# Kernel optimization log

Measured on AMD Instinct MI355X. Metric: run time of the kernel, lower is better.

The kernel has to match this reference:

```python
import jax, jax.numpy as jnp
import numpy as np

N_HEADS = 16
NOPE = 128
ROPE = 64
VDIM = 128
HEAD_DIM = NOPE + ROPE  # 192


def apply_rope(x, cos, sin):
    # x: [B, S, H, D] with D even; pairs (a, b) rotated by complex freqs.
    B, S, H, D = x.shape
    xr = x.reshape(B, S, H, D // 2, 2)
    a, b = xr[..., 0], xr[..., 1]
    c = cos[None, :, None, :]
    s = sin[None, :, None, :]
    out = jnp.stack([a * c - b * s, a * s + b * c], axis=-1)
    return out.reshape(B, S, H, D)


def setup_inputs() -> dict:
    key = jax.random.key(0)
    ks = jax.random.split(key, 8)
    B, S, DIM = 1, 2048, 2048
    x = jax.random.normal(ks[0], (B, S, DIM), dtype=jnp.float32)
    wq = jax.random.normal(ks[1], (N_HEADS * HEAD_DIM, DIM), dtype=jnp.float32) * (DIM ** -0.5)
    wk = jax.random.normal(ks[2], (N_HEADS * HEAD_DIM, DIM), dtype=jnp.float32) * (DIM ** -0.5)
    wv = jax.random.normal(ks[3], (N_HEADS * VDIM, DIM), dtype=jnp.float32) * (DIM ** -0.5)
    wo = jax.random.normal(ks[4], (DIM, N_HEADS * VDIM), dtype=jnp.float32) * ((N_HEADS * VDIM) ** -0.5)
    # rotary freqs: theta = 10000^{-2i/d}, angles = pos * theta
    inv_freq = 1.0 / (10000.0 ** (np.arange(0, ROPE, 2, dtype=np.float32) / ROPE))
    angles = np.arange(S, dtype=np.float32)[:, None] * inv_freq[None, :]  # [S, 32]
    freqs_cos = jnp.asarray(np.cos(angles))
    freqs_sin = jnp.asarray(np.sin(angles))
    # additive causal mask
    mask = jnp.where(jnp.triu(jnp.ones((S, S), dtype=bool), k=1), -1e9, 0.0).astype(jnp.float32)
    return {"x": x, "wq": wq, "wk": wk, "wv": wv, "wo": wo,
            "freqs_cos": freqs_cos, "freqs_sin": freqs_sin, "mask": mask, "start_pos": 0}


def reference(x, wq, wk, wv, wo, freqs_cos, freqs_sin, mask, start_pos):
    B, S, DIM = x.shape
    q = (x @ wq.T).reshape(B, S, N_HEADS, HEAD_DIM)
    k = (x @ wk.T).reshape(B, S, N_HEADS, HEAD_DIM)
    v = (x @ wv.T).reshape(B, S, N_HEADS, VDIM)
    q_nope, q_pe = q[..., :NOPE], q[..., NOPE:]
    k_nope, k_pe = k[..., :NOPE], k[..., NOPE:]
    q_pe = apply_rope(q_pe, freqs_cos, freqs_sin)
    k_pe = apply_rope(k_pe, freqs_cos, freqs_sin)
    scores = (jnp.einsum('bshd,bthd->bsht', q_nope, k_nope)
              + jnp.einsum('bshd,bthd->bsht', q_pe, k_pe)) * (HEAD_DIM ** -0.5)
    scores = scores + mask[None, :, None, :]
    probs = jax.nn.softmax(scores.astype(jnp.float32), axis=-1).astype(x.dtype)
    out = jnp.einsum('bsht,bthd->bshd', probs, v)
    return out.reshape(B, S, N_HEADS * VDIM) @ wo.T
```

## Files before the change

### kernel.cpp

```cpp
#include <hip/hip_runtime.h>
#include <hip/hip_bf16.h>
#include <math.h>

#define NH 16
#define NOPE 128
#define ROPE 64
#define VDIM 128
#define HD 192
#define SEQ 2048
#define DIM 2048
#define QKD (NH * HD)
#define VD  (NH * VDIM)
#define QKVS 8192

typedef __attribute__((ext_vector_type(8))) short short8;
typedef __attribute__((ext_vector_type(4))) short short4v;
typedef __attribute__((ext_vector_type(4))) float f32x4;
typedef unsigned int u32;

#define WAIT_VM8  0x0F78
#define WAIT_VM6  0x0F76
#define WAIT_VM4  0x0F74
#define WAIT_VM0  0x0F70
#define WAIT_LGKM 0xC07F

static __device__ inline short f2bf(float f) {
  union { float f; unsigned u; } v; v.f = f;
  unsigned r = (v.u + 0x7fffu + ((v.u >> 16) & 1u)) >> 16;
  return (short)r;
}
static __device__ inline float bf2f(unsigned short u) {
  union { unsigned u; float f; } v; v.u = ((unsigned)u) << 16;
  return v.f;
}

static __device__ __forceinline__ void gload16(const short* g, short* l) {
  __builtin_amdgcn_global_load_lds(
      (const __attribute__((address_space(1))) u32*)g,
      (__attribute__((address_space(3))) u32*)l, 16, 0, 0);
}


#define RDA(pp, hh, mh) do { \
  const char* Lb_ = Lsm + ((pp) * 32768) + ((hh) * 16384) + aoff; \
  afr[0] = *(const short8*)(Lb_ + ((mh) * 4096) + 0); \
  afr[1] = *(const short8*)(Lb_ + ((mh) * 4096) + 1024); \
  afr[2] = *(const short8*)(Lb_ + ((mh) * 4096) + 2048); \
  afr[3] = *(const short8*)(Lb_ + ((mh) * 4096) + 3072); \
} while (0)

#define RDB(pp, hh) do { \
  const char* Lb_ = Lsm + 65536 + ((pp) * 32768) + ((hh) * 16384) + boff; \
  bfr[0] = *(const short8*)(Lb_ + 0); \
  bfr[1] = *(const short8*)(Lb_ + 1024); \
  bfr[2] = *(const short8*)(Lb_ + 2048); \
  bfr[3] = *(const short8*)(Lb_ + 3072); \
} while (0)

#define SA(kt, h) do { \
  char* d_ = Lsm + (((kt) & 1) * 32768) + ((h) * 16384) + wv * 1024; \
  gload16(gA0 + (kt) * 64 + (h) * 32, (short*)d_); \
  gload16(gA1 + (kt) * 64 + (h) * 32, (short*)(d_ + 8192)); \
} while (0)

#define SB(kt, h) do { \
  char* d_ = Lsm + 65536 + (((kt) & 1) * 32768) + ((h) * 16384) + wv * 1024; \
  gload16(gB0 + (kt) * 64 + (h) * 32, (short*)d_); \
  gload16(gB1 + (kt) * 64 + (h) * 32, (short*)(d_ + 8192)); \
} while (0)

#define MFMA1(mi, ni) \
  acc[mi][ni] = __builtin_amdgcn_mfma_f32_16x16x32_bf16(afr[(mi) & 3], bfr[ni], acc[mi][ni], 0, 0, 0)

#define MM(mh) do { \
  MFMA1((mh)*4+0, 0); MFMA1((mh)*4+1, 0); MFMA1((mh)*4+2, 0); MFMA1((mh)*4+3, 0); \
  MFMA1((mh)*4+0, 1); MFMA1((mh)*4+1, 1); MFMA1((mh)*4+2, 1); MFMA1((mh)*4+3, 1); \
  MFMA1((mh)*4+0, 2); MFMA1((mh)*4+1, 2); MFMA1((mh)*4+2, 2); MFMA1((mh)*4+3, 2); \
  MFMA1((mh)*4+0, 3); MFMA1((mh)*4+1, 3); MFMA1((mh)*4+2, 3); MFMA1((mh)*4+3, 3); \
} while (0)

#define GBAR() __builtin_amdgcn_s_barrier()
#define GLGKM0() __builtin_amdgcn_s_waitcnt(WAIT_LGKM)
#define GPRIO1() __builtin_amdgcn_s_setprio(1)
#define GPRIO0() __builtin_amdgcn_s_setprio(0)
#define GNOP ((void)0)

#define TILE(pp, S1, S2, S3, S4, VMW) do { \
  RDA(pp, 0, 0); RDB(pp, 0); S1; \
  GBAR(); GLGKM0(); GPRIO1(); MM(0); GPRIO0(); GBAR(); \
  RDA(pp, 0, 1); S2; \
  GBAR(); GLGKM0(); GPRIO1(); MM(1); GPRIO0(); GBAR(); \
  RDA(pp, 1, 0); RDB(pp, 1); S3; \
  GBAR(); GLGKM0(); GPRIO1(); MM(0); GPRIO0(); GBAR(); \
  RDA(pp, 1, 1); S4; \
  GBAR(); GLGKM0(); GPRIO1(); MM(1); GPRIO0(); VMW; GBAR(); \
} while (0)

__global__ __launch_bounds__(512, 2) void gemm256_bt(
    const short* __restrict__ A, const short* __restrict__ B,
    short* __restrict__ C, int K, int lda, int ldb, int ldc) {
  __shared__ __align__(16) char Lsm[131072];

  const int tid = threadIdx.x;
  const int lane = tid & 63;
  const int l15 = lane & 15;
  const int quad = lane >> 4;
  const int wv = tid >> 6;
  const int wr = wv >> 2, wc = wv & 3;

  const int bid = blockIdx.x;
  const int swz = (bid & 7) * 32 + (bid >> 3);
  const int m0 = (swz >> 5) * 256;
  const int n0 = (swz & 31) * 256;

  const short* gA0 = A + (size_t)(m0 + wv * 16 + l15) * lda + quad * 8;
  const short* gA1 = gA0 + (size_t)128 * lda;
  const short* gB0 = B + (size_t)(n0 + wv * 16 + l15) * ldb + quad * 8;
  const short* gB1 = gB0 + (size_t)128 * ldb;

  const int aoff = wr * 8192 + lane * 16;
  const int boff = wc * 4096 + lane * 16;

  f32x4 acc[8][4];
#pragma unroll
  for (int i = 0; i < 8; ++i)
#pragma unroll
    for (int j = 0; j < 4; ++j) acc[i][j] = (f32x4)(0.f);
  short8 afr[4], bfr[4];

  const int NT = K >> 6;

  SB(0, 0); SA(0, 0); SB(0, 1); SA(0, 1);
  SB(1, 0); SA(1, 0); SB(1, 1);
  __builtin_amdgcn_s_waitcnt(WAIT_VM6);
  GBAR();

  int kt = 0;
  for (; kt + 4 <= NT; kt += 2) {
    TILE(0, SA(kt + 1, 1), SB(kt + 2, 0), SA(kt + 2, 0), SB(kt + 2, 1),
         __builtin_amdgcn_s_waitcnt(WAIT_VM6));
    TILE(1, SA(kt + 2, 1), SB(kt + 3, 0), SA(kt + 3, 0), SB(kt + 3, 1),
         __builtin_amdgcn_s_waitcnt(WAIT_VM6));
  }
  TILE(0, SA(kt + 1, 1), GNOP, GNOP, GNOP, __builtin_amdgcn_s_waitcnt(WAIT_VM0));
  TILE(1, GNOP, GNOP, GNOP, GNOP, GNOP);

#pragma unroll
  for (int m = 0; m < 8; ++m) {
    const size_t rb = (size_t)(m0 + wr * 128 + m * 16 + quad * 4) * ldc +
                      n0 + wc * 64 + l15;
#pragma unroll
    for (int n = 0; n < 4; ++n)
#pragma unroll
      for (int r = 0; r < 4; ++r)
        C[rb + (size_t)r * ldc + n * 16] = f2bf(acc[m][n][r]);
  }
}

template <bool BF16OUT>
__global__ __launch_bounds__(256) void gemm_bt(
    const short* __restrict__ A, const short* __restrict__ B,
    void* __restrict__ Cv, int K, int lda, int ldb, int ldc, float oscale) {
  __shared__ __align__(16) short Ls[4][2][4096];

  const int tid = threadIdx.x;
  const int lane = tid & 63;
  const int wave = tid >> 6;
  const int wr = wave >> 1, wc = wave & 1;
  const int lane15 = lane & 15, quad = lane >> 4;
  const int m0 = blockIdx.y * 128, n0 = blockIdx.x * 128;

  const short* gA[4]; const short* gB[4];
#pragma unroll
  for (int i = 0; i < 4; ++i) {
    int gidx = i * 64 + lane;
    int r = gidx >> 2, p = gidx & 3;
    int g = (p ^ ((r >> 1) & 3)) * 8;
    gA[i] = A + (size_t)(m0 + wr * 64 + r) * lda + g;
    gB[i] = B + (size_t)(n0 + wc * 64 + r) * ldb + g;
  }

  f32x4 acc[4][4];
#pragma unroll
  for (int i = 0; i < 4; ++i)
#pragma unroll
    for (int j = 0; j < 4; ++j) acc[i][j] = (f32x4)(0.f);

#pragma unroll
  for (int i = 0; i < 4; ++i) gload16(gA[i], &Ls[wave][0][i * 512]);
#pragma unroll
  for (int i = 0; i < 4; ++i) gload16(gB[i], &Ls[wave][0][2048 + i * 512]);

  const int rsw = (lane15 >> 1) & 3;
  for (int k0 = 0; k0 < K; k0 += 32) {
    const int cur = (k0 >> 5) & 1;
    __builtin_amdgcn_s_waitcnt(WAIT_LGKM);
    if (k0 + 32 < K) {
      const int nxt = cur ^ 1;
#pragma unroll
      for (int i = 0; i < 4; ++i) gload16(gA[i] + k0 + 32, &Ls[wave][nxt][i * 512]);
#pragma unroll
      for (int i = 0; i < 4; ++i) gload16(gB[i] + k0 + 32, &Ls[wave][nxt][2048 + i * 512]);
      __builtin_amdgcn_s_waitcnt(WAIT_VM8);
    } else {
      __builtin_amdgcn_s_waitcnt(WAIT_VM0);
    }
    const short* bufp = &Ls[wave][cur][0];
    short8 af[4], bfv[4];
#pragma unroll
    for (int i = 0; i < 4; ++i)
      af[i] = *(const short8*)&bufp[(i * 16 + lane15) * 32 + (quad ^ rsw) * 8];
#pragma unroll
    for (int j = 0; j < 4; ++j)
      bfv[j] = *(const short8*)&bufp[2048 + (j * 16 + lane15) * 32 + (quad ^ rsw) * 8];
#pragma unroll
    for (int i = 0; i < 4; ++i)
#pragma unroll
      for (int j = 0; j < 4; ++j)
        acc[i][j] = __builtin_amdgcn_mfma_f32_16x16x32_bf16(af[i], bfv[j], acc[i][j], 0, 0, 0);
  }

#pragma unroll
  for (int i = 0; i < 4; ++i)
#pragma unroll
    for (int j = 0; j < 4; ++j)
#pragma unroll
      for (int r = 0; r < 4; ++r) {
        size_t idx = (size_t)(m0 + wr * 64 + i * 16 + quad * 4 + r) * ldc +
                     n0 + wc * 64 + j * 16 + lane15;
        if (BF16OUT)
          ((short*)Cv)[idx] = f2bf(acc[i][j][r] * oscale);
        else
          ((float*)Cv)[idx] = acc[i][j][r];
      }
}

__global__ __launch_bounds__(256) void rope_qk(
    short* __restrict__ qk, const float* __restrict__ cosf, const float* __restrict__ sinf) {
  int idx = blockIdx.x * blockDim.x + threadIdx.x;
  int j = idx & 31;
  int h = (idx >> 5) & (NH - 1);
  int s = idx >> 9;
  if (s >= SEQ) return;

  float c = cosf[s * 32 + j];
  float sn = sinf[s * 32 + j];
  size_t rowb = (size_t)s * QKVS + h * HD + NOPE + 2 * j;

  u32* pq = (u32*)(qk + rowb);
  u32 w = *pq;
  float a = bf2f((unsigned short)(w & 0xffff));
  float b = bf2f((unsigned short)(w >> 16));
  *pq = (u32)(unsigned short)f2bf(a * c - b * sn) |
        ((u32)(unsigned short)f2bf(a * sn + b * c) << 16);

  u32* pk = (u32*)(qk + rowb + QKD);
  w = *pk;
  a = bf2f((unsigned short)(w & 0xffff));
  b = bf2f((unsigned short)(w >> 16));
  *pk = (u32)(unsigned short)f2bf(a * c - b * sn) |
        ((u32)(unsigned short)f2bf(a * sn + b * c) << 16);
}

__global__ __launch_bounds__(256) void bf16_convert(
    const float* __restrict__ in, short* __restrict__ out, int n4) {
  int i = blockIdx.x * 256 + threadIdx.x;
  if (i >= n4) return;
  float4 f = ((const float4*)in)[i];
  short4v o;
  o.x = f2bf(f.x); o.y = f2bf(f.y); o.z = f2bf(f.z); o.w = f2bf(f.w);
  ((short4v*)out)[i] = o;
}

__global__ __launch_bounds__(256) void conv_wqkv(
    const float* __restrict__ wq, const float* __restrict__ wk,
    const float* __restrict__ wv, short* __restrict__ wqkv, int n4) {
  int i = blockIdx.x * 256 + threadIdx.x;
  if (i >= n4) return;
  int row = i >> 9;
  float4 f;
  if (row < QKD) f = ((const float4*)wq)[i];
  else if (row < 2 * QKD) f = ((const float4*)wk)[i - QKD * (DIM / 4)];
  else f = ((const float4*)wv)[i - 2 * QKD * (DIM / 4)];
  short4v o;
  o.x = f2bf(f.x); o.y = f2bf(f.y); o.z = f2bf(f.z); o.w = f2bf(f.w);
  ((short4v*)wqkv)[i] = o;
}

__global__ __launch_bounds__(256) void vt_bf16(
    const short* __restrict__ vb, short* __restrict__ vtb) {
  __shared__ short tile[64][74];
  const int t0 = blockIdx.x * 64;
  const int c0 = blockIdx.y * 64;
  const int tid = threadIdx.x;
#pragma unroll
  for (int i = 0; i < 16; ++i) {
    int idx = i * 256 + tid;
    int r = idx >> 6, c = idx & 63;
    tile[r][c] = vb[(size_t)(t0 + r) * QKVS + c0 + c];
  }
  __syncthreads();
  const int h = c0 >> 7;
  const int dbase = c0 & 127;
#pragma unroll
  for (int i = 0; i < 16; ++i) {
    int idx = i * 256 + tid;
    int d = idx >> 6, t = idx & 63;
    vtb[(size_t)h * VDIM * SEQ + (size_t)(dbase + d) * SEQ + t0 + t] = tile[t][d];
  }
}

#define BQ 64
#define BT 64
#define CHT 8
#define PSTR 76
#define MFIX 8.0f

__global__ __launch_bounds__(256) void attn_part(
    const short* __restrict__ qk,
    const short* __restrict__ vtb,
    short* __restrict__ Opart,
    float* __restrict__ lpart)
{
  __shared__ __align__(16) short Ks[2][BT * 192];
  __shared__ __align__(16) short Vt[VDIM * 64];
  __shared__ __align__(16) short Ps[4 * 16 * PSTR];

  const int bid = blockIdx.x;
  const int i0 = bid >> 3;
  const int h = (bid & 7) + ((i0 >> 7) << 3);
  const int qt = (i0 & 127) >> 2;
  const int chk = i0 & 3;
  if (chk * CHT > qt) return;

  const int tid = threadIdx.x;
  const int wave = tid >> 6;
  const int lane = tid & 63;
  const int lane15 = lane & 15;
  const int quad = lane >> 4;
  const int bb = qt >> 3;
  const int slot = h * 80 + qt + 4 * bb * (bb - 1) + (qt - 8 * bb) * bb + chk;
  const int R0 = qt * BQ;
  const int kt_beg = chk * CHT;
  const int kt_end = min(kt_beg + CHT, qt + 1);
  const float scale = 0.072168784f;

  const int qrow = R0 + wave * 16 + lane15;
  short8 qf[6];
  const short* qbase = qk + (size_t)qrow * QKVS + h * HD + quad * 8;
#pragma unroll
  for (int kc = 0; kc < 6; ++kc) qf[kc] = *(const short8*)(qbase + kc * 32);
  __builtin_amdgcn_sched_barrier(0);

  const short* kb = qk + QKD;
  int lKoff[6]; const short* gK[6];
#pragma unroll
  for (int i = 0; i < 6; ++i) {
    int id = i * 256 + tid;
    int row = id / 24, cX = id - row * 24;
    int ch = cX ^ (row & 7);
    lKoff[i] = id * 8;
    gK[i] = kb + (size_t)row * QKVS + h * HD + ch * 8;
  }
  const short* gV[4]; short* lV[4];
#pragma unroll
  for (int i = 0; i < 4; ++i) {
    int id = i * 256 + tid;
    int row = id >> 3, cX = id & 7;
    int ch = cX ^ (row & 7);
    lV[i] = &Vt[id * 8];
    gV[i] = vtb + (size_t)h * VDIM * SEQ + (size_t)row * SEQ + ch * 8;
  }

  f32x4 oacc[8];
#pragma unroll
  for (int i = 0; i < 8; ++i) oacc[i] = (f32x4)(0.f);
  float lsum[4] = {0.f, 0.f, 0.f, 0.f};

  short* pw = &Ps[wave * 16 * PSTR];

  {
    const size_t t0 = (size_t)kt_beg * BT;
#pragma unroll
    for (int i = 0; i < 6; ++i) gload16(gK[i] + t0 * QKVS, &Ks[0][lKoff[i]]);
#pragma unroll
    for (int i = 0; i < 4; ++i) gload16(gV[i] + t0, lV[i]);
  }
  __builtin_amdgcn_s_waitcnt(WAIT_VM0);
  __builtin_amdgcn_s_barrier();
  __builtin_amdgcn_sched_barrier(0);

  for (int kt = kt_beg; kt < kt_end; ++kt) {
    const int cur = (kt - kt_beg) & 1;
    const bool have = (kt + 1 < kt_end);

    if (have) {
      const size_t tn = (size_t)(kt + 1) * BT;
#pragma unroll
      for (int i = 0; i < 6; ++i) gload16(gK[i] + tn * QKVS, &Ks[cur ^ 1][lKoff[i]]);
    }

    const short* kcur = &Ks[cur][0];
    f32x4 sacc[4];
    __builtin_amdgcn_s_setprio(1);
#pragma unroll
    for (int c = 0; c < 4; ++c) {
      sacc[c] = (f32x4)(0.f);
      const int row = c * 16 + lane15;
#pragma unroll
      for (int kc = 0; kc < 6; ++kc) {
        int cX = (4 * kc + quad) ^ (lane15 & 7);
        short8 kf = *(const short8*)&kcur[row * 192 + cX * 8];
        sacc[c] = __builtin_amdgcn_mfma_f32_16x16x32_bf16(qf[kc], kf, sacc[c], 0, 0, 0);
      }
    }
    __builtin_amdgcn_s_setprio(0);

    if (kt == qt) {
#pragma unroll
      for (int c = 0; c < 4; ++c)
#pragma unroll
        for (int r = 0; r < 4; ++r) {
          int tloc = c * 16 + lane15;
          int qloc = wave * 16 + quad * 4 + r;
          if (tloc > qloc) sacc[c][r] = -1e30f;
        }
    }

#pragma unroll
    for (int c = 0; c < 4; ++c)
#pragma unroll
      for (int r = 0; r < 4; ++r) {
        float p = __expf(sacc[c][r] * scale - MFIX);
        lsum[r] += p;
        pw[(quad * 4 + r) * PSTR + c * 16 + lane15] = f2bf(p);
      }

    short8 pf0 = *(const short8*)&pw[lane15 * PSTR + quad * 8];
    short8 pf1 = *(const short8*)&pw[lane15 * PSTR + 32 + quad * 8];

    if (have) __builtin_amdgcn_s_waitcnt(WAIT_VM6);
    else      __builtin_amdgcn_s_waitcnt(WAIT_VM0);
    __builtin_amdgcn_s_barrier();
    __builtin_amdgcn_sched_barrier(0);

    __builtin_amdgcn_s_setprio(1);
#pragma unroll
    for (int ch = 0; ch < 8; ++ch) {
      const int row = ch * 16 + lane15;
      int cX0 = quad ^ (lane15 & 7);
      int cX1 = (4 + quad) ^ (lane15 & 7);
      short8 vf0 = *(const short8*)&Vt[row * 64 + cX0 * 8];
      short8 vf1 = *(const short8*)&Vt[row * 64 + cX1 * 8];
      oacc[ch] = __builtin_amdgcn_mfma_f32_16x16x32_bf16(pf0, vf0, oacc[ch], 0, 0, 0);
      oacc[ch] = __builtin_amdgcn_mfma_f32_16x16x32_bf16(pf1, vf1, oacc[ch], 0, 0, 0);
    }
    __builtin_amdgcn_s_setprio(0);

    if (have) {
      __builtin_amdgcn_s_waitcnt(WAIT_LGKM);
      __builtin_amdgcn_s_barrier();
      const size_t tn = (size_t)(kt + 1) * BT;
#pragma unroll
      for (int i = 0; i < 4; ++i) gload16(gV[i] + tn, lV[i]);
      __builtin_amdgcn_s_waitcnt(WAIT_VM4);
      __builtin_amdgcn_s_barrier();
      __builtin_amdgcn_sched_barrier(0);
    }
  }

  short* op = Opart + (size_t)slot * (64 * 128);
#pragma unroll
  for (int ch = 0; ch < 8; ++ch)
#pragma unroll
    for (int r = 0; r < 4; ++r)
      op[(wave * 16 + quad * 4 + r) * 128 + ch * 16 + lane15] = f2bf(oacc[ch][r]);

  float red[4];
#pragma unroll
  for (int r = 0; r < 4; ++r) {
    float s = lsum[r];
    s += __shfl_xor(s, 1, 64);
    s += __shfl_xor(s, 2, 64);
    s += __shfl_xor(s, 4, 64);
    s += __shfl_xor(s, 8, 64);
    red[r] = s;
  }
  if (lane15 == 0) {
#pragma unroll
    for (int r = 0; r < 4; ++r)
      lpart[(size_t)slot * 64 + wave * 16 + quad * 4 + r] = red[r];
  }
}

__global__ __launch_bounds__(256) void attn_combine(
    const short* __restrict__ Opart, const float* __restrict__ lpart,
    short* __restrict__ aob) {
  const int qt = blockIdx.x, h = blockIdx.y;
  const int nact = (qt >> 3) + 1;
  const int bb = qt >> 3;
  const int base = h * 80 + qt + 4 * bb * (bb - 1) + (qt - 8 * bb) * bb;
  const int tid = threadIdx.x;
  const int row = tid >> 2;
  const int cg = (tid & 3) * 32;

  float acc[32];
#pragma unroll
  for (int e = 0; e < 32; ++e) acc[e] = 0.f;
  float lsum = 0.f;

  for (int c = 0; c < nact; ++c) {
    const short* sp = Opart + (size_t)(base + c) * (64 * 128) + row * 128 + cg;
    lsum += lpart[(size_t)(base + c) * 64 + row];
#pragma unroll
    for (int g = 0; g < 4; ++g) {
      short8 vv = *(const short8*)(sp + g * 8);
#pragma unroll
      for (int e = 0; e < 8; ++e) acc[g * 8 + e] += bf2f((unsigned short)vv[e]);
    }
  }

  float inv = 1.f / lsum;
#pragma unroll
  for (int g = 0; g < 4; ++g) {
    short8 ov;
#pragma unroll
    for (int e = 0; e < 8; ++e) ov[e] = f2bf(acc[g * 8 + e] * inv);
    *(short8*)(aob + (size_t)(qt * 64 + row) * QKVS + h * 128 + cg + g * 8) = ov;
  }
}

extern "C" void kernel_launch(void* const* d_in, const int* in_sizes, int n_in,
                              void* d_out, int out_size, void* d_ws, size_t ws_size,
                              hipStream_t stream) {
  const float* x  = (const float*)d_in[0];
  const float* wq = (const float*)d_in[1];
  const float* wk = (const float*)d_in[2];
  const float* wv = (const float*)d_in[3];
  const float* wo = (const float*)d_in[4];
  const float* fc = (const float*)d_in[5];
  const float* fs = (const float*)d_in[6];

  char* ws8 = (char*)d_ws;
  short* xb    = (short*)(ws8 + 0);
  short* wo_b  = (short*)(ws8 + 0);
  short* wqkv  = (short*)(ws8 + 8388608);
  short* vtb   = (short*)(ws8 + 8388608);
  short* Opart = (short*)(ws8 + 16777216);
  float* lpart = (float*)(ws8 + 37748736);
  short* qkv   = (short*)(ws8 + 41943040);
  float* out   = (float*)d_out;

  const int NX4 = DIM * DIM / 4;
  const int NQKV4 = QKVS * DIM / 4;
  const int ROPE_GRID = (SEQ * NH * 32) / 256;

  bf16_convert<<<(NX4 + 255) / 256, 256, 0, stream>>>(x, xb, NX4);
  conv_wqkv<<<(NQKV4 + 255) / 256, 256, 0, stream>>>(wq, wk, wv, wqkv, NQKV4);

  gemm256_bt<<<dim3((QKVS / 256) * (SEQ / 256)), 512, 0, stream>>>(
      xb, wqkv, qkv, DIM, DIM, DIM, QKVS);
  rope_qk<<<ROPE_GRID, 256, 0, stream>>>(qkv, fc, fs);
  vt_bf16<<<dim3(SEQ / 64, VD / 64), 256, 0, stream>>>(qkv + 2 * QKD, vtb);

  bf16_convert<<<(NX4 + 255) / 256, 256, 0, stream>>>(wo, wo_b, NX4);

  attn_part<<<dim3(2048), 256, 0, stream>>>(qkv, vtb, Opart, lpart);
  attn_combine<<<dim3(SEQ / BQ, NH), 256, 0, stream>>>(Opart, lpart, qkv + 2 * QKD);

  gemm_bt<false><<<dim3(DIM / 128, SEQ / 128), 256, 0, stream>>>(
      qkv + 2 * QKD, wo_b, out, DIM, QKVS, DIM, DIM, 1.0f);
}
```

Before: 351.0 us.

## Load V directly into registers, single-buffer K, and raise occupancy

The attention-partial kernel no longer stages V through LDS. Each wave loads its V fragments from global memory straight into registers, and K drops from double to single buffering, with the next K prefetch issued after the QK MFMAs finish. Launch bounds now request 3 blocks per SM, and query tiles are visited in reverse order so the heaviest causal tiles start first. The aim is to cut LDS use and barriers so more blocks fit per CU. The cost is more VGPRs, and less overlap between the K load and compute, since the next K load must wait for the current tile's use to finish.

```diff
diff --git a/kernel.cpp b/kernel.cpp
--- a/kernel.cpp
+++ b/kernel.cpp
@@ -18,9 +18,9 @@
 typedef __attribute__((ext_vector_type(4))) float f32x4;
 typedef unsigned int u32;
 
+#define WAIT_VM16 0x4F70
 #define WAIT_VM8  0x0F78
 #define WAIT_VM6  0x0F76
-#define WAIT_VM4  0x0F74
 #define WAIT_VM0  0x0F70
 #define WAIT_LGKM 0xC07F
 
@@ -316,20 +316,19 @@
 #define PSTR 76
 #define MFIX 8.0f
 
-__global__ __launch_bounds__(256) void attn_part(
+__global__ __launch_bounds__(256, 3) void attn_part(
     const short* __restrict__ qk,
     const short* __restrict__ vtb,
     short* __restrict__ Opart,
     float* __restrict__ lpart)
 {
-  __shared__ __align__(16) short Ks[2][BT * 192];
-  __shared__ __align__(16) short Vt[VDIM * 64];
+  __shared__ __align__(16) short Ks[BT * 192];
   __shared__ __align__(16) short Ps[4 * 16 * PSTR];
 
   const int bid = blockIdx.x;
   const int i0 = bid >> 3;
   const int h = (bid & 7) + ((i0 >> 7) << 3);
-  const int qt = (i0 & 127) >> 2;
+  const int qt = 31 - ((i0 & 127) >> 2);
   const int chk = i0 & 3;
   if (chk * CHT > qt) return;
 
@@ -362,45 +361,34 @@
     lKoff[i] = id * 8;
     gK[i] = kb + (size_t)row * QKVS + h * HD + ch * 8;
   }
-  const short* gV[4]; short* lV[4];
-#pragma unroll
-  for (int i = 0; i < 4; ++i) {
-    int id = i * 256 + tid;
-    int row = id >> 3, cX = id & 7;
-    int ch = cX ^ (row & 7);
-    lV[i] = &Vt[id * 8];
-    gV[i] = vtb + (size_t)h * VDIM * SEQ + (size_t)row * SEQ + ch * 8;
-  }
+
+  const short* vbase = vtb + ((size_t)(h * VDIM + lane15) * SEQ) + quad * 8;
 
   f32x4 oacc[8];
 #pragma unroll
   for (int i = 0; i < 8; ++i) oacc[i] = (f32x4)(0.f);
   float lsum[4] = {0.f, 0.f, 0.f, 0.f};
+  short8 vreg[8][2];
 
   short* pw = &Ps[wave * 16 * PSTR];
 
   {
     const size_t t0 = (size_t)kt_beg * BT;
 #pragma unroll
-    for (int i = 0; i < 6; ++i) gload16(gK[i] + t0 * QKVS, &Ks[0][lKoff[i]]);
-#pragma unroll
-    for (int i = 0; i < 4; ++i) gload16(gV[i] + t0, lV[i]);
-  }
-  __builtin_amdgcn_s_waitcnt(WAIT_VM0);
+    for (int i = 0; i < 6; ++i) gload16(gK[i] + t0 * QKVS, &Ks[lKoff[i]]);
+#pragma unroll
+    for (int ch = 0; ch < 8; ++ch)
+#pragma unroll
+      for (int hf = 0; hf < 2; ++hf)
+        vreg[ch][hf] = *(const short8*)(vbase + (size_t)ch * 16 * SEQ + t0 + hf * 32);
+  }
+  __builtin_amdgcn_s_waitcnt(WAIT_VM16);
   __builtin_amdgcn_s_barrier();
   __builtin_amdgcn_sched_barrier(0);
 
   for (int kt = kt_beg; kt < kt_end; ++kt) {
-    const int cur = (kt - kt_beg) & 1;
     const bool have = (kt + 1 < kt_end);
 
-    if (have) {
-      const size_t tn = (size_t)(kt + 1) * BT;
-#pragma unroll
-      for (int i = 0; i < 6; ++i) gload16(gK[i] + tn * QKVS, &Ks[cur ^ 1][lKoff[i]]);
-    }
-
-    const short* kcur = &Ks[cur][0];
     f32x4 sacc[4];
     __builtin_amdgcn_s_setprio(1);
 #pragma unroll
@@ -410,11 +398,20 @@
 #pragma unroll
       for (int kc = 0; kc < 6; ++kc) {
         int cX = (4 * kc + quad) ^ (lane15 & 7);
-        short8 kf = *(const short8*)&kcur[row * 192 + cX * 8];
+        short8 kf = *(const short8*)&Ks[row * 192 + cX * 8];
         sacc[c] = __builtin_amdgcn_mfma_f32_16x16x32_bf16(qf[kc], kf, sacc[c], 0, 0, 0);
       }
     }
     __builtin_amdgcn_s_setprio(0);
+
+    __builtin_amdgcn_s_barrier();
+    __builtin_amdgcn_sched_barrier(0);
+
+    if (have) {
+      const size_t tn = (size_t)(kt + 1) * BT;
+#pragma unroll
+      for (int i = 0; i < 6; ++i) gload16(gK[i] + tn * QKVS, &Ks[lKoff[i]]);
+    }
 
     if (kt == qt) {
 #pragma unroll
@@ -441,29 +438,25 @@
 
     if (have) __builtin_amdgcn_s_waitcnt(WAIT_VM6);
     else      __builtin_amdgcn_s_waitcnt(WAIT_VM0);
-    __builtin_amdgcn_s_barrier();
     __builtin_amdgcn_sched_barrier(0);
 
     __builtin_amdgcn_s_setprio(1);
 #pragma unroll
     for (int ch = 0; ch < 8; ++ch) {
-      const int row = ch * 16 + lane15;
-      int cX0 = quad ^ (lane15 & 7);
-      int cX1 = (4 + quad) ^ (lane15 & 7);
-      short8 vf0 = *(const short8*)&Vt[row * 64 + cX0 * 8];
-      short8 vf1 = *(const short8*)&Vt[row * 64 + cX1 * 8];
-      oacc[ch] = __builtin_amdgcn_mfma_f32_16x16x32_bf16(pf0, vf0, oacc[ch], 0, 0, 0);
-      oacc[ch] = __builtin_amdgcn_mfma_f32_16x16x32_bf16(pf1, vf1, oacc[ch], 0, 0, 0);
+      oacc[ch] = __builtin_amdgcn_mfma_f32_16x16x32_bf16(pf0, vreg[ch][0], oacc[ch], 0, 0, 0);
+      oacc[ch] = __builtin_amdgcn_mfma_f32_16x16x32_bf16(pf1, vreg[ch][1], oacc[ch], 0, 0, 0);
     }
     __builtin_amdgcn_s_setprio(0);
+    __builtin_amdgcn_sched_barrier(0);
 
     if (have) {
-      __builtin_amdgcn_s_waitcnt(WAIT_LGKM);
-      __builtin_amdgcn_s_barrier();
       const size_t tn = (size_t)(kt + 1) * BT;
 #pragma unroll
-      for (int i = 0; i < 4; ++i) gload16(gV[i] + tn, lV[i]);
-      __builtin_amdgcn_s_waitcnt(WAIT_VM4);
+      for (int ch = 0; ch < 8; ++ch)
+#pragma unroll
+        for (int hf = 0; hf < 2; ++hf)
+          vreg[ch][hf] = *(const short8*)(vbase + (size_t)ch * 16 * SEQ + tn + hf * 32);
+      __builtin_amdgcn_s_waitcnt(WAIT_VM16);
       __builtin_amdgcn_s_barrier();
       __builtin_amdgcn_sched_barrier(0);
     }
```

Measured after the change: 424.8 us. +21.1%, slower.
